# Optimization experiments

Hardware: AMD Instinct MI355X
Metric: run time of the kernel (lower is better)

## Reference

```python
import jax, jax.numpy as jnp
import numpy as np

B, H, F = 4096, 32, 1024     # batch, hp_num, feat_dim
N_CAT, CAT_DIM = 8, 16       # categorical dims 0..7, each |domain| = 16
N_CONT = H - N_CAT
LN_EPS = 1e-5


def setup_inputs() -> dict:
    key = jax.random.key(0)
    ks = jax.random.split(key, 8)
    s = 1.0 / np.sqrt(F)  # ~xavier scale
    return {
        "z": jax.random.normal(ks[0], (B, F), jnp.float32),
        "edge": jax.random.randint(ks[1], (2, 10), 0, B),
        # stacked per-hp projection Linears (weights stored as [in, out])
        "W_proj": jax.random.normal(ks[2], (H, F, F), jnp.float32) * s,
        "b_proj": jnp.zeros((H, F), jnp.float32),
        # LayerNorm over [hp_num, feat_dim]
        "ln_w": jnp.ones((H, F), jnp.float32),
        "ln_b": jnp.zeros((H, F), jnp.float32),
        # reverse_embedding for categorical dims (softmax heads)
        "W_cat": jax.random.normal(ks[3], (N_CAT, F, CAT_DIM), jnp.float32) * s,
        "b_cat": jnp.zeros((N_CAT, CAT_DIM), jnp.float32),
        # reverse_embedding for continuous dims (scalar heads)
        "W_cont": jax.random.normal(ks[4], (N_CONT, F, 1), jnp.float32) * s,
        "b_cont": jnp.zeros((N_CONT, 1), jnp.float32),
    }


def reference(z, edge, W_proj, b_proj, ln_w, ln_b, W_cat, b_cat, W_cont, b_cont):
    # per-hp projection: batched GEMM replacing batch*hp_num tiny Linears
    latent = jnp.einsum('bf,hfd->bhd', z, W_proj) + b_proj  # [B, H, F]
    # LayerNorm normalized over the last two dims [hp_num, feat_dim]
    mu = latent.mean(axis=(1, 2), keepdims=True)
    var = latent.var(axis=(1, 2), keepdims=True)
    latent = (latent - mu) * jax.lax.rsqrt(var + LN_EPS) * ln_w + ln_b
    latent = jax.nn.relu(latent)
    # reverse embeddings: categorical heads (dims 0..N_CAT-1) get softmax
    cat_logits = jnp.einsum('bhf,hfc->bhc', latent[:, :N_CAT], W_cat) + b_cat
    pred_cat = jax.nn.softmax(cat_logits, axis=-1)          # [B, N_CAT, CAT_DIM]
    pred_cont = jnp.einsum('bhf,hfc->bhc', latent[:, N_CAT:], W_cont) + b_cont  # [B, N_CONT, 1]
    return pred_cat, pred_cont, latent
```

## Files before the change

### kernel.cpp

```cpp
#include <hip/hip_runtime.h>

typedef unsigned short u16;
typedef __bf16 bf16x8 __attribute__((ext_vector_type(8)));
typedef float f32x4 __attribute__((ext_vector_type(4)));

#define B_SZ   4096
#define H_NUM  32
#define F_DIM  1024
#define NTOT   (H_NUM * F_DIM)
#define N_CAT  8
#define CAT_D  16
#define N_CONT 24
#define LN_EPS 1e-5f
#define NSTRIP 128

__device__ __forceinline__ u16 f2bf(float f) {
    unsigned int u = __builtin_bit_cast(unsigned int, f);
    unsigned int r = (u + 0x7FFFu + ((u >> 16) & 1u)) >> 16;
    return (u16)r;
}

__device__ __forceinline__ float bf2f(u16 v) {
    unsigned int u = ((unsigned int)v) << 16;
    return __builtin_bit_cast(float, u);
}

__device__ __forceinline__ void gl2lds16(const void* g, void* l) {
    __builtin_amdgcn_global_load_lds(
        (const __attribute__((address_space(1))) void*)g,
        (__attribute__((address_space(3))) void*)l,
        16, 0, 0);
}

__device__ __forceinline__ float wave_sum(float v) {
#pragma unroll
    for (int o = 32; o; o >>= 1) v += __shfl_xor(v, o);
    return v;
}

__global__ __launch_bounds__(256) void zconv(const float* __restrict__ z,
                                             u16* __restrict__ zb) {
    int i = blockIdx.x * 256 + threadIdx.x;
    float4 v = ((const float4*)z)[i];
    ushort4 o;
    o.x = f2bf(v.x); o.y = f2bf(v.y); o.z = f2bf(v.z); o.w = f2bf(v.w);
    ((ushort4*)zb)[i] = o;
}

__global__ __launch_bounds__(256) void transpose_w(const float* __restrict__ W,
                                                   u16* __restrict__ Wt) {
    __shared__ u16 tile[64][72];
    const int h = blockIdx.z;
    const int f0 = blockIdx.x * 64;
    const int d0 = blockIdx.y * 64;
    const float* Wh = W + (size_t)h * F_DIM * F_DIM;
    u16* Wth = Wt + (size_t)h * F_DIM * F_DIM;
    const int t = threadIdx.x;

#pragma unroll
    for (int i = 0; i < 4; ++i) {
        int idx = i * 256 + t;
        int fr = idx >> 4;
        int c4 = idx & 15;
        float4 v = *(const float4*)(Wh + (size_t)(f0 + fr) * F_DIM + d0 + c4 * 4);
        tile[fr][c4 * 4 + 0] = f2bf(v.x);
        tile[fr][c4 * 4 + 1] = f2bf(v.y);
        tile[fr][c4 * 4 + 2] = f2bf(v.z);
        tile[fr][c4 * 4 + 3] = f2bf(v.w);
    }
    __syncthreads();
#pragma unroll
    for (int i = 0; i < 2; ++i) {
        int idx = i * 256 + t;
        int dr = idx >> 3;
        int c8 = idx & 7;
        __attribute__((aligned(16))) u16 tmp[8];
#pragma unroll
        for (int j = 0; j < 8; ++j) tmp[j] = tile[c8 * 8 + j][dr];
        *(uint4*)(Wth + (size_t)(d0 + dr) * F_DIM + f0 + c8 * 8) = *(const uint4*)tmp;
    }
}

template <int BF>
__global__ __launch_bounds__(512, 2) void gemm256(const u16* __restrict__ A,
                                                  const u16* __restrict__ Bt,
                                                  const float* __restrict__ bproj,
                                                  u16* __restrict__ lat16,
                                                  float* __restrict__ latf,
                                                  float* __restrict__ psum,
                                                  float* __restrict__ psumsq) {
    extern __shared__ u16 dynlds[];
    const int t = threadIdx.x;
    const int wid = t >> 6;
    const int lane = t & 63;
    const int l16 = lane & 15;
    const int lk = lane >> 4;
    const int wm = wid >> 2;
    const int wn = wid & 3;

    const int wg = blockIdx.x;
    const int xcd = wg & 7;
    const int local = wg >> 3;
    const int m0 = (local & 15) * 256;
    const int n0 = ((xcd << 4) + (local >> 4)) * 256;

    f32x4 acc[8][4];
    const f32x4 zero = {0.f, 0.f, 0.f, 0.f};
#pragma unroll
    for (int m = 0; m < 8; ++m)
#pragma unroll
        for (int n = 0; n < 4; ++n) acc[m][n] = zero;

    auto stage = [&](int p, int ktn, int bn) {
        const char* srcbase = (p < 2) ? (const char*)A : (const char*)Bt;
        const int rowbase = (p < 2) ? (m0 + p * 128) : (n0 + (p - 2) * 128);
        u16* ldsbase = dynlds + bn * 32768 + (p >> 1) * 16384 + (p & 1) * 8192;
#pragma unroll
        for (int i = 0; i < 2; ++i) {
            int oo = i * 8192 + t * 16;
            int oos = oo ^ (((oo >> 7) & 7) << 4);
            int row = oo >> 7;
            int colb = oos & 127;
            gl2lds16(srcbase + (size_t)(rowbase + row) * 2048 + ktn * 128 + colb,
                     ldsbase + i * 4096 + (wid << 9));
        }
    };

#pragma unroll
    for (int p = 0; p < 4; ++p) stage(p, 0, 0);
    __syncthreads();

    const int swz = (l16 & 7) << 4;
    for (int kt = 0; kt < 16; ++kt) {
        const int buf = kt & 1;
        const char* aB = (const char*)(dynlds + buf * 32768 + wm * 8192);
        const char* bB = (const char*)(dynlds + buf * 32768 + 16384 + (wn >> 1) * 8192);
        bf16x8 bfr[4][2];
#pragma unroll
        for (int p = 0; p < 4; ++p) {
            if (kt < 15) stage(p, kt + 1, buf ^ 1);
            if (p == 0) {
#pragma unroll
                for (int nr = 0; nr < 4; ++nr)
#pragma unroll
                    for (int kk = 0; kk < 2; ++kk)
                        bfr[nr][kk] = *(const bf16x8*)(bB +
                            ((wn & 1) * 64 + nr * 16 + l16) * 128 +
                            ((kk * 64 + lk * 16) ^ swz));
            }
            bf16x8 afr[2][2];
#pragma unroll
            for (int mr = 0; mr < 2; ++mr)
#pragma unroll
                for (int kk = 0; kk < 2; ++kk)
                    afr[mr][kk] = *(const bf16x8*)(aB +
                        (p * 32 + mr * 16 + l16) * 128 +
                        ((kk * 64 + lk * 16) ^ swz));
            __builtin_amdgcn_s_setprio(1);
#pragma unroll
            for (int kk = 0; kk < 2; ++kk)
#pragma unroll
                for (int mr = 0; mr < 2; ++mr)
#pragma unroll
                    for (int nr = 0; nr < 4; ++nr)
                        acc[p * 2 + mr][nr] = __builtin_amdgcn_mfma_f32_16x16x32_bf16(
                            afr[mr][kk], bfr[nr][kk], acc[p * 2 + mr][nr], 0, 0, 0);
            __builtin_amdgcn_s_setprio(0);
        }
        __syncthreads();
    }

    float bias[4];
#pragma unroll
    for (int nr = 0; nr < 4; ++nr) bias[nr] = bproj[n0 + wn * 64 + nr * 16 + l16];

    float sm[8][4], s2[8][4];
#pragma unroll
    for (int mr = 0; mr < 8; ++mr)
#pragma unroll
        for (int j = 0; j < 4; ++j) { sm[mr][j] = 0.f; s2[mr][j] = 0.f; }

#pragma unroll
    for (int mr = 0; mr < 8; ++mr) {
#pragma unroll
        for (int j = 0; j < 4; ++j) {
            const int rowg = m0 + wm * 128 + mr * 16 + lk * 4 + j;
            size_t off = (size_t)rowg * NTOT + n0 + wn * 64 + l16;
#pragma unroll
            for (int nr = 0; nr < 4; ++nr) {
                float v = acc[mr][nr][j] + bias[nr];
                if (BF) lat16[off + nr * 16] = f2bf(v);
                else    latf[off + nr * 16] = v;
                sm[mr][j] += v;
                s2[mr][j] += v * v;
            }
        }
    }
#pragma unroll
    for (int o = 1; o < 16; o <<= 1) {
#pragma unroll
        for (int mr = 0; mr < 8; ++mr)
#pragma unroll
            for (int j = 0; j < 4; ++j) {
                sm[mr][j] += __shfl_xor(sm[mr][j], o);
                s2[mr][j] += __shfl_xor(s2[mr][j], o);
            }
    }
    float* sredf = (float*)dynlds;
    float* s2f   = sredf + 1024;
    __syncthreads();
    if (l16 == 0) {
#pragma unroll
        for (int mr = 0; mr < 8; ++mr)
#pragma unroll
            for (int j = 0; j < 4; ++j) {
                int r = wm * 128 + mr * 16 + lk * 4 + j;
                sredf[wn * 256 + r] = sm[mr][j];
                s2f[wn * 256 + r] = s2[mr][j];
            }
    }
    __syncthreads();
    if (t < 256) {
        const int strip = n0 >> 8;
        float S = sredf[t] + sredf[256 + t] + sredf[512 + t] + sredf[768 + t];
        float S2 = s2f[t] + s2f[256 + t] + s2f[512 + t] + s2f[768 + t];
        psum[(size_t)strip * B_SZ + m0 + t] = S;
        psumsq[(size_t)strip * B_SZ + m0 + t] = S2;
    }
}

__global__ __launch_bounds__(256) void ln_finalize(const float* __restrict__ psum,
                                                   const float* __restrict__ psumsq,
                                                   float* __restrict__ murs) {
    const int t = threadIdx.x;
    const int b0 = blockIdx.x * 64;
    const int tb = t & 63;
    const int tg = t >> 6;
    float s = 0.f, s2 = 0.f;
    for (int sidx = tg; sidx < NSTRIP; sidx += 4) {
        s += psum[(size_t)sidx * B_SZ + b0 + tb];
        s2 += psumsq[(size_t)sidx * B_SZ + b0 + tb];
    }
    __shared__ float r1[4][64], r2[4][64];
    r1[tg][tb] = s;
    r2[tg][tb] = s2;
    __syncthreads();
    if (t < 64) {
        float S = r1[0][t] + r1[1][t] + r1[2][t] + r1[3][t];
        float S2 = r2[0][t] + r2[1][t] + r2[2][t] + r2[3][t];
        float m = S / (float)NTOT;
        float var = S2 / (float)NTOT - m * m;
        murs[b0 + t] = m;
        murs[B_SZ + b0 + t] = rsqrtf(var + LN_EPS);
    }
}

template <int BF>
__global__ __launch_bounds__(256) void headsH(const void* __restrict__ latin_,
                                              float* __restrict__ latout,
                                              const float* __restrict__ murs,
                                              const float* __restrict__ lnw,
                                              const float* __restrict__ lnb,
                                              const float* __restrict__ Wcat,
                                              const float* __restrict__ bcat,
                                              const float* __restrict__ Wcont,
                                              const float* __restrict__ bcont,
                                              float* __restrict__ pcat,
                                              float* __restrict__ pcont) {
    const int b = blockIdx.x;
    const int t = threadIdx.x;
    const int lane = t & 63;
    const int w4 = t >> 6;
    const float mu = murs[b];
    const float rs = murs[B_SZ + b];
    const ushort4* lin16 = (const ushort4*)((const u16*)latin_ + (size_t)b * NTOT);
    const float4*  linf  = (const float4*)((const float*)latin_ + (size_t)b * NTOT);
    float4* lout4 = (float4*)(latout + (size_t)b * NTOT);
    const float4* lnw4 = (const float4*)lnw;
    const float4* lnb4 = (const float4*)lnb;
    const float4* wcont4 = (const float4*)Wcont;

    __shared__ ushort4 sy16[N_CAT * 256];
    __shared__ float cred[4][N_CAT][CAT_D];
    __shared__ float nred[N_CONT][4];

#pragma unroll 2
    for (int k = 0; k < N_CAT; ++k) {
        const int i = (k << 8) + t;
        float4 x;
        if (BF) {
            ushort4 xv = lin16[i];
            x.x = bf2f(xv.x); x.y = bf2f(xv.y); x.z = bf2f(xv.z); x.w = bf2f(xv.w);
        } else {
            x = linf[i];
        }
        float4 w = lnw4[i];
        float4 bv = lnb4[i];
        float4 yo;
        yo.x = fmaxf(0.f, (x.x - mu) * rs * w.x + bv.x);
        yo.y = fmaxf(0.f, (x.y - mu) * rs * w.y + bv.y);
        yo.z = fmaxf(0.f, (x.z - mu) * rs * w.z + bv.z);
        yo.w = fmaxf(0.f, (x.w - mu) * rs * w.w + bv.w);
        lout4[i] = yo;
        ushort4 ys;
        ys.x = f2bf(yo.x); ys.y = f2bf(yo.y); ys.z = f2bf(yo.z); ys.w = f2bf(yo.w);
        sy16[i] = ys;
    }

    float cp[N_CONT];
#pragma unroll 2
    for (int k = N_CAT; k < H_NUM; ++k) {
        const int i = (k << 8) + t;
        float4 x;
        if (BF) {
            ushort4 xv = lin16[i];
            x.x = bf2f(xv.x); x.y = bf2f(xv.y); x.z = bf2f(xv.z); x.w = bf2f(xv.w);
        } else {
            x = linf[i];
        }
        float4 w = lnw4[i];
        float4 bv = lnb4[i];
        float4 wv = wcont4[((k - N_CAT) << 8) + t];
        float4 yo;
        yo.x = fmaxf(0.f, (x.x - mu) * rs * w.x + bv.x);
        yo.y = fmaxf(0.f, (x.y - mu) * rs * w.y + bv.y);
        yo.z = fmaxf(0.f, (x.z - mu) * rs * w.z + bv.z);
        yo.w = fmaxf(0.f, (x.w - mu) * rs * w.w + bv.w);
        lout4[i] = yo;
        cp[k - N_CAT] = yo.x * wv.x + yo.y * wv.y + yo.z * wv.z + yo.w * wv.w;
    }
    __syncthreads();

    const int c = t & 15;
    const int g = t >> 4;
    for (int k = 0; k < N_CAT; ++k) {
        const float* Wc = Wcat + (size_t)k * F_DIM * CAT_D + c;
        float acc = 0.f;
#pragma unroll
        for (int j = 0; j < 16; ++j) {
            ushort4 yv = sy16[(k << 8) + g * 16 + j];
            int fb = (g * 64 + j * 4) * CAT_D;
            acc += bf2f(yv.x) * Wc[fb] + bf2f(yv.y) * Wc[fb + CAT_D] +
                   bf2f(yv.z) * Wc[fb + 2 * CAT_D] + bf2f(yv.w) * Wc[fb + 3 * CAT_D];
        }
        acc += __shfl_xor(acc, 16);
        acc += __shfl_xor(acc, 32);
        if (lane < 16) cred[w4][k][lane] = acc;
    }
#pragma unroll
    for (int k = 0; k < N_CONT; ++k) {
        float v = wave_sum(cp[k]);
        if (lane == 0) nred[k][w4] = v;
    }
    __syncthreads();

    if (t < 128) {
        const int h = t >> 4, cc = t & 15;
        float lg = cred[0][h][cc] + cred[1][h][cc] + cred[2][h][cc] + cred[3][h][cc] +
                   bcat[h * CAT_D + cc];
        float mx = lg;
#pragma unroll
        for (int o = 8; o; o >>= 1) mx = fmaxf(mx, __shfl_xor(mx, o, 16));
        float e = __expf(lg - mx);
        float sm2 = e;
#pragma unroll
        for (int o = 8; o; o >>= 1) sm2 += __shfl_xor(sm2, o, 16);
        pcat[(size_t)b * (N_CAT * CAT_D) + t] = e / sm2;
    } else if (t >= 128 && t < 128 + N_CONT) {
        const int ci = t - 128;
        pcont[(size_t)b * N_CONT + ci] =
            nred[ci][0] + nred[ci][1] + nred[ci][2] + nred[ci][3] + bcont[ci];
    }
}

extern "C" void kernel_launch(void* const* d_in, const int* in_sizes, int n_in,
                              void* d_out, int out_size, void* d_ws, size_t ws_size,
                              hipStream_t stream) {
    const float* z     = (const float*)d_in[0];
    const float* Wp    = (const float*)d_in[2];
    const float* bp    = (const float*)d_in[3];
    const float* lnw   = (const float*)d_in[4];
    const float* lnb   = (const float*)d_in[5];
    const float* Wcat  = (const float*)d_in[6];
    const float* bcat  = (const float*)d_in[7];
    const float* Wcont = (const float*)d_in[8];
    const float* bcont = (const float*)d_in[9];

    float* out    = (float*)d_out;
    float* pcat   = out;
    float* pcont  = out + (size_t)B_SZ * N_CAT * CAT_D;
    float* latent = pcont + (size_t)B_SZ * N_CONT;

    u16* zb     = (u16*)d_ws;
    u16* Wt     = zb + (size_t)B_SZ * F_DIM;
    float* murs = (float*)(Wt + (size_t)NTOT * F_DIM);
    float* psum   = murs + 2 * B_SZ;
    float* psumsq = psum + (size_t)B_SZ * NSTRIP;
    u16* lat16  = (u16*)(psumsq + (size_t)B_SZ * NSTRIP);

    const size_t need = (size_t)((char*)(lat16 + (size_t)B_SZ * NTOT) - (char*)d_ws);
    const bool usebf = ws_size >= need;

    const int LDSB = 131072;
    zconv<<<dim3(B_SZ * F_DIM / 1024), 256, 0, stream>>>(z, zb);
    transpose_w<<<dim3(16, 16, 32), 256, 0, stream>>>(Wp, Wt);
    if (usebf) {
        (void)hipFuncSetAttribute((const void*)gemm256<1>,
                                  hipFuncAttributeMaxDynamicSharedMemorySize, LDSB);
        gemm256<1><<<dim3(2048), 512, LDSB, stream>>>(zb, Wt, bp, lat16, nullptr,
                                                      psum, psumsq);
        ln_finalize<<<dim3(B_SZ / 64), 256, 0, stream>>>(psum, psumsq, murs);
        headsH<1><<<dim3(B_SZ), 256, 0, stream>>>(lat16, latent, murs, lnw, lnb,
                                                  Wcat, bcat, Wcont, bcont, pcat, pcont);
    } else {
        (void)hipFuncSetAttribute((const void*)gemm256<0>,
                                  hipFuncAttributeMaxDynamicSharedMemorySize, LDSB);
        gemm256<0><<<dim3(2048), 512, LDSB, stream>>>(zb, Wt, bp, nullptr, latent,
                                                      psum, psumsq);
        ln_finalize<<<dim3(B_SZ / 64), 256, 0, stream>>>(psum, psumsq, murs);
        headsH<0><<<dim3(B_SZ), 256, 0, stream>>>(latent, latent, murs, lnw, lnb,
                                                  Wcat, bcat, Wcont, bcont, pcat, pcont);
    }
}
```

Measured before the change: 745.7 us.

## Split heads kernel across two blocks per row with nontemporal latent stores

The heads kernel now launches two blocks per batch row, each handling 16 of the 32 hp slices. This doubles the number of blocks and spreads the per-row work. The latent output is written with nontemporal stores to avoid polluting the cache. The categorical GEMV is restructured so each thread reads float4 weight vectors and reduces with shuffles. The cost is a divergent first half that alone carries the categorical softmax work, which unbalances the two blocks.

```diff
diff --git a/kernel.cpp b/kernel.cpp
--- a/kernel.cpp
+++ b/kernel.cpp
@@ -256,7 +256,7 @@
 }
 
 template <int BF>
-__global__ __launch_bounds__(256) void headsH(const void* __restrict__ latin_,
+__global__ __launch_bounds__(256) void headsI(const void* __restrict__ latin_,
                                               float* __restrict__ latout,
                                               const float* __restrict__ murs,
                                               const float* __restrict__ lnw,
@@ -267,7 +267,8 @@
                                               const float* __restrict__ bcont,
                                               float* __restrict__ pcat,
                                               float* __restrict__ pcont) {
-    const int b = blockIdx.x;
+    const int half = blockIdx.x;
+    const int b = blockIdx.y;
     const int t = threadIdx.x;
     const int lane = t & 63;
     const int w4 = t >> 6;
@@ -275,17 +276,21 @@
     const float rs = murs[B_SZ + b];
     const ushort4* lin16 = (const ushort4*)((const u16*)latin_ + (size_t)b * NTOT);
     const float4*  linf  = (const float4*)((const float*)latin_ + (size_t)b * NTOT);
-    float4* lout4 = (float4*)(latout + (size_t)b * NTOT);
+    f32x4* lout4 = (f32x4*)(latout + (size_t)b * NTOT);
     const float4* lnw4 = (const float4*)lnw;
     const float4* lnb4 = (const float4*)lnb;
     const float4* wcont4 = (const float4*)Wcont;
 
     __shared__ ushort4 sy16[N_CAT * 256];
-    __shared__ float cred[4][N_CAT][CAT_D];
-    __shared__ float nred[N_CONT][4];
-
-#pragma unroll 2
-    for (int k = 0; k < N_CAT; ++k) {
+    __shared__ float4 cred4[4][N_CAT][4];
+    __shared__ float nred[16][4];
+
+    const int kbase = half << 4;
+    float cp[16];
+
+#pragma unroll 4
+    for (int kk = 0; kk < 16; ++kk) {
+        const int k = kbase + kk;
         const int i = (k << 8) + t;
         float4 x;
         if (BF) {
@@ -301,75 +306,89 @@
         yo.y = fmaxf(0.f, (x.y - mu) * rs * w.y + bv.y);
         yo.z = fmaxf(0.f, (x.z - mu) * rs * w.z + bv.z);
         yo.w = fmaxf(0.f, (x.w - mu) * rs * w.w + bv.w);
-        lout4[i] = yo;
-        ushort4 ys;
-        ys.x = f2bf(yo.x); ys.y = f2bf(yo.y); ys.z = f2bf(yo.z); ys.w = f2bf(yo.w);
-        sy16[i] = ys;
-    }
-
-    float cp[N_CONT];
-#pragma unroll 2
-    for (int k = N_CAT; k < H_NUM; ++k) {
-        const int i = (k << 8) + t;
-        float4 x;
-        if (BF) {
-            ushort4 xv = lin16[i];
-            x.x = bf2f(xv.x); x.y = bf2f(xv.y); x.z = bf2f(xv.z); x.w = bf2f(xv.w);
+        f32x4 yv = {yo.x, yo.y, yo.z, yo.w};
+        __builtin_nontemporal_store(yv, lout4 + i);
+        if (half == 0 && k < N_CAT) {
+            ushort4 ys;
+            ys.x = f2bf(yo.x); ys.y = f2bf(yo.y); ys.z = f2bf(yo.z); ys.w = f2bf(yo.w);
+            sy16[i] = ys;
+            cp[kk] = 0.f;
         } else {
-            x = linf[i];
-        }
-        float4 w = lnw4[i];
-        float4 bv = lnb4[i];
-        float4 wv = wcont4[((k - N_CAT) << 8) + t];
-        float4 yo;
-        yo.x = fmaxf(0.f, (x.x - mu) * rs * w.x + bv.x);
-        yo.y = fmaxf(0.f, (x.y - mu) * rs * w.y + bv.y);
-        yo.z = fmaxf(0.f, (x.z - mu) * rs * w.z + bv.z);
-        yo.w = fmaxf(0.f, (x.w - mu) * rs * w.w + bv.w);
-        lout4[i] = yo;
-        cp[k - N_CAT] = yo.x * wv.x + yo.y * wv.y + yo.z * wv.z + yo.w * wv.w;
-    }
-    __syncthreads();
-
-    const int c = t & 15;
-    const int g = t >> 4;
-    for (int k = 0; k < N_CAT; ++k) {
-        const float* Wc = Wcat + (size_t)k * F_DIM * CAT_D + c;
-        float acc = 0.f;
-#pragma unroll
-        for (int j = 0; j < 16; ++j) {
-            ushort4 yv = sy16[(k << 8) + g * 16 + j];
-            int fb = (g * 64 + j * 4) * CAT_D;
-            acc += bf2f(yv.x) * Wc[fb] + bf2f(yv.y) * Wc[fb + CAT_D] +
-                   bf2f(yv.z) * Wc[fb + 2 * CAT_D] + bf2f(yv.w) * Wc[fb + 3 * CAT_D];
-        }
-        acc += __shfl_xor(acc, 16);
-        acc += __shfl_xor(acc, 32);
-        if (lane < 16) cred[w4][k][lane] = acc;
-    }
-#pragma unroll
-    for (int k = 0; k < N_CONT; ++k) {
-        float v = wave_sum(cp[k]);
-        if (lane == 0) nred[k][w4] = v;
-    }
-    __syncthreads();
-
-    if (t < 128) {
-        const int h = t >> 4, cc = t & 15;
-        float lg = cred[0][h][cc] + cred[1][h][cc] + cred[2][h][cc] + cred[3][h][cc] +
-                   bcat[h * CAT_D + cc];
-        float mx = lg;
-#pragma unroll
-        for (int o = 8; o; o >>= 1) mx = fmaxf(mx, __shfl_xor(mx, o, 16));
-        float e = __expf(lg - mx);
-        float sm2 = e;
-#pragma unroll
-        for (int o = 8; o; o >>= 1) sm2 += __shfl_xor(sm2, o, 16);
-        pcat[(size_t)b * (N_CAT * CAT_D) + t] = e / sm2;
-    } else if (t >= 128 && t < 128 + N_CONT) {
-        const int ci = t - 128;
-        pcont[(size_t)b * N_CONT + ci] =
-            nred[ci][0] + nred[ci][1] + nred[ci][2] + nred[ci][3] + bcont[ci];
+            float4 wv = wcont4[((k - N_CAT) << 8) + t];
+            cp[kk] = yo.x * wv.x + yo.y * wv.y + yo.z * wv.z + yo.w * wv.w;
+        }
+    }
+    __syncthreads();
+
+    if (half == 0) {
+        const int cq = t & 3;
+        const int fg = t >> 2;
+        for (int k = 0; k < N_CAT; ++k) {
+            const float4* Wc4 = (const float4*)(Wcat + (size_t)k * F_DIM * CAT_D);
+            float4 a4 = {0.f, 0.f, 0.f, 0.f};
+#pragma unroll
+            for (int jq = 0; jq < 4; ++jq) {
+                ushort4 yv = sy16[(k << 8) + fg * 4 + jq];
+                float ys[4] = {bf2f(yv.x), bf2f(yv.y), bf2f(yv.z), bf2f(yv.w)};
+#pragma unroll
+                for (int r = 0; r < 4; ++r) {
+                    int f = fg * 16 + jq * 4 + r;
+                    float4 wv = Wc4[f * 4 + cq];
+                    a4.x += ys[r] * wv.x;
+                    a4.y += ys[r] * wv.y;
+                    a4.z += ys[r] * wv.z;
+                    a4.w += ys[r] * wv.w;
+                }
+            }
+#pragma unroll
+            for (int o = 4; o < 64; o <<= 1) {
+                a4.x += __shfl_xor(a4.x, o);
+                a4.y += __shfl_xor(a4.y, o);
+                a4.z += __shfl_xor(a4.z, o);
+                a4.w += __shfl_xor(a4.w, o);
+            }
+            if (lane < 4) cred4[w4][k][lane] = a4;
+        }
+#pragma unroll
+        for (int kk = 8; kk < 16; ++kk) {
+            float v = wave_sum(cp[kk]);
+            if (lane == 0) nred[kk - 8][w4] = v;
+        }
+    } else {
+#pragma unroll
+        for (int kk = 0; kk < 16; ++kk) {
+            float v = wave_sum(cp[kk]);
+            if (lane == 0) nred[kk][w4] = v;
+        }
+    }
+    __syncthreads();
+
+    if (half == 0) {
+        if (t < 128) {
+            const int h = t >> 4, c = t & 15;
+            float lg = bcat[h * CAT_D + c];
+#pragma unroll
+            for (int w = 0; w < 4; ++w)
+                lg += ((const float*)cred4[w][h])[c];
+            float mx = lg;
+#pragma unroll
+            for (int o = 8; o; o >>= 1) mx = fmaxf(mx, __shfl_xor(mx, o, 16));
+            float e = __expf(lg - mx);
+            float sm2 = e;
+#pragma unroll
+            for (int o = 8; o; o >>= 1) sm2 += __shfl_xor(sm2, o, 16);
+            pcat[(size_t)b * (N_CAT * CAT_D) + t] = e / sm2;
+        } else if (t >= 128 && t < 128 + 8) {
+            const int ci = t - 128;
+            pcont[(size_t)b * N_CONT + ci] =
+                nred[ci][0] + nred[ci][1] + nred[ci][2] + nred[ci][3] + bcont[ci];
+        }
+    } else {
+        if (t < 16) {
+            const int ci = 8 + t;
+            pcont[(size_t)b * N_CONT + ci] =
+                nred[t][0] + nred[t][1] + nred[t][2] + nred[t][3] + bcont[ci];
+        }
     }
 }
 
@@ -410,15 +429,15 @@
         gemm256<1><<<dim3(2048), 512, LDSB, stream>>>(zb, Wt, bp, lat16, nullptr,
                                                       psum, psumsq);
         ln_finalize<<<dim3(B_SZ / 64), 256, 0, stream>>>(psum, psumsq, murs);
-        headsH<1><<<dim3(B_SZ), 256, 0, stream>>>(lat16, latent, murs, lnw, lnb,
-                                                  Wcat, bcat, Wcont, bcont, pcat, pcont);
+        headsI<1><<<dim3(2, B_SZ), 256, 0, stream>>>(lat16, latent, murs, lnw, lnb,
+                                                     Wcat, bcat, Wcont, bcont, pcat, pcont);
     } else {
         (void)hipFuncSetAttribute((const void*)gemm256<0>,
                                   hipFuncAttributeMaxDynamicSharedMemorySize, LDSB);
         gemm256<0><<<dim3(2048), 512, LDSB, stream>>>(zb, Wt, bp, nullptr, latent,
                                                       psum, psumsq);
         ln_finalize<<<dim3(B_SZ / 64), 256, 0, stream>>>(psum, psumsq, murs);
-        headsH<0><<<dim3(B_SZ), 256, 0, stream>>>(latent, latent, murs, lnw, lnb,
-                                                  Wcat, bcat, Wcont, bcont, pcat, pcont);
-    }
-}
+        headsI<0><<<dim3(2, B_SZ), 256, 0, stream>>>(latent, latent, murs, lnw, lnb,
+                                                     Wcat, bcat, Wcont, bcont, pcat, pcont);
+    }
+}
```

After: 777.7 us. +4.3%, slower.
